# Performance work log

Measured on AMD Instinct MI355X. Metric: run time of the kernel, lower is better.

Reference implementation:

```python
import jax, jax.numpy as jnp
import numpy as np

B, S, D, H = 2, 2048, 1024, 16
HD = D // H  # 64


def setup_inputs() -> dict:
    key = jax.random.key(0)
    ks = jax.random.split(key, 7)
    std = 1.0 / np.sqrt(D)
    return {
        "q": jax.random.normal(ks[0], (B, S, D), jnp.float32),
        "k": jax.random.normal(ks[1], (B, S, D), jnp.float32),
        "v": jax.random.normal(ks[2], (B, S, D), jnp.float32),
        "w_q": jax.random.normal(ks[3], (D, D), jnp.float32) * std,
        "w_k": jax.random.normal(ks[4], (D, D), jnp.float32) * std,
        "w_v": jax.random.normal(ks[5], (D, D), jnp.float32) * std,
        "w_o": jax.random.normal(ks[6], (D, D), jnp.float32) * std,
    }


def reference(q, k, v, w_q, w_k, w_v, w_o):
    # Linear (torch nn.Linear, no bias): y = x @ W.T
    Q = jnp.einsum('bsd,ed->bse', q, w_q)
    K = jnp.einsum('bsd,ed->bse', k, w_k)
    V = jnp.einsum('bsd,ed->bse', v, w_v)
    # split heads -> (B, H, S, HD)
    Qh = Q.reshape(B, S, H, HD).transpose(0, 2, 1, 3)
    Kh = K.reshape(B, S, H, HD).transpose(0, 2, 1, 3)
    Vh = V.reshape(B, S, H, HD).transpose(0, 2, 1, 3)
    scale = 1.0 / np.sqrt(HD).astype(np.float32)
    scores = jnp.einsum('bhqd,bhkd->bhqk', Qh, Kh) * scale  # [B,H,S,S]
    attn = jax.nn.softmax(scores, axis=-1)
    ctx = jnp.einsum('bhqk,bhkd->bhqd', attn, Vh)
    combined = ctx.transpose(0, 2, 1, 3).reshape(B, S, D)
    out = jnp.einsum('bsd,ed->bse', combined, w_o)
    return out, attn
```

## Files before the change

### kernel.cpp

```cpp
#include <hip/hip_runtime.h>
#include <hip/hip_bf16.h>
#include <cstdint>

#define B_ 2
#define S_ 2048
#define D_ 1024
#define H_ 16
#define HD_ 64

#define SCALE_LOG2 0.18033688011112042f

typedef __attribute__((ext_vector_type(8))) __bf16 bf16x8;
typedef __attribute__((ext_vector_type(8))) unsigned short ushort8;
typedef __attribute__((ext_vector_type(4))) unsigned short ushort4v;
typedef __attribute__((ext_vector_type(4))) float f32x4;

__device__ __forceinline__ unsigned short f2bf(float f) {
  __bf16 h = (__bf16)f;
  return __builtin_bit_cast(unsigned short, h);
}

__device__ __forceinline__ float bf2f(unsigned short u) {
  union { unsigned int i; float f; } v; v.i = ((unsigned int)u) << 16; return v.f;
}

__device__ __forceinline__ float fexp2(float x) {
#if __has_builtin(__builtin_amdgcn_exp2f)
  return __builtin_amdgcn_exp2f(x);
#else
  return exp2f(x);
#endif
}

__device__ __forceinline__ f32x4 mfma16(bf16x8 a, bf16x8 b, f32x4 c) {
  return __builtin_amdgcn_mfma_f32_16x16x32_bf16(a, b, c, 0, 0, 0);
}

#define LGKM_BARRIER()                                        \
  do {                                                        \
    asm volatile("s_waitcnt lgkmcnt(0)" ::: "memory");        \
    __builtin_amdgcn_s_barrier();                             \
  } while (0)

__global__ __launch_bounds__(256) void proj_qkv_kernel(
    const float* __restrict__ qin, const float* __restrict__ kin,
    const float* __restrict__ vin, const float* __restrict__ wq,
    const float* __restrict__ wk, const float* __restrict__ wv,
    unsigned short* __restrict__ qh, unsigned short* __restrict__ kh,
    unsigned short* __restrict__ vt)
{
  __shared__ unsigned short As[128][40];
  __shared__ unsigned short Bs[128][40];

  const int z = blockIdx.z;
  const float* X = (z == 0) ? qin : (z == 1) ? kin : vin;
  const float* W = (z == 0) ? wq : (z == 1) ? wk : wv;
  unsigned short* dst = (z == 0) ? qh : (z == 1) ? kh : vt;
  const float osc = (z == 0) ? SCALE_LOG2 : 1.0f;

  const int lin = blockIdx.x + 8 * blockIdx.y;
  const int swz = (lin & 7) * 32 + (lin >> 3);
  const int bx = swz & 7, by = swz >> 3;

  const int tid = threadIdx.x;
  const int lane = tid & 63, wid = tid >> 6;
  const int c = lane & 15, g = lane >> 4;
  const int wr = wid >> 1, wc = wid & 1;
  const int m0 = by * 128, n0 = bx * 128;

  const int sr = tid >> 1, sh = tid & 1;
  const float* Ap = X + (size_t)(m0 + sr) * D_ + sh * 16;
  const float* Bp = W + (size_t)(n0 + sr) * D_ + sh * 16;

  float ar[16], br[16];
  f32x4 acc[4][4];
#pragma unroll
  for (int i = 0; i < 4; ++i)
#pragma unroll
    for (int j = 0; j < 4; ++j) acc[i][j] = (f32x4){0.f, 0.f, 0.f, 0.f};

  auto ldg_tile = [&](int kt) {
    const float* ap = Ap + kt * 32;
    const float* bp = Bp + kt * 32;
#pragma unroll
    for (int j = 0; j < 4; ++j) {
      *(f32x4*)(ar + 4 * j) = *(const f32x4*)(ap + 4 * j);
      *(f32x4*)(br + 4 * j) = *(const f32x4*)(bp + 4 * j);
    }
  };
  auto sts_tile = [&]() {
    unsigned short ta[16], tb[16];
#pragma unroll
    for (int j = 0; j < 16; ++j) { ta[j] = f2bf(ar[j]); tb[j] = f2bf(br[j]); }
    *(ushort8*)&As[sr][sh * 16]     = *(ushort8*)&ta[0];
    *(ushort8*)&As[sr][sh * 16 + 8] = *(ushort8*)&ta[8];
    *(ushort8*)&Bs[sr][sh * 16]     = *(ushort8*)&tb[0];
    *(ushort8*)&Bs[sr][sh * 16 + 8] = *(ushort8*)&tb[8];
  };

  ldg_tile(0);
  sts_tile();
  __syncthreads();

  for (int kt = 0; kt < 32; ++kt) {
    if (kt < 31) ldg_tile(kt + 1);
    bf16x8 af[4], bfr[4];
#pragma unroll
    for (int i = 0; i < 4; ++i) af[i]  = *(bf16x8*)&As[wr * 64 + i * 16 + c][g * 8];
#pragma unroll
    for (int i = 0; i < 4; ++i) bfr[i] = *(bf16x8*)&Bs[wc * 64 + i * 16 + c][g * 8];
#pragma unroll
    for (int mi = 0; mi < 4; ++mi)
#pragma unroll
      for (int ni = 0; ni < 4; ++ni)
        acc[mi][ni] = mfma16(af[mi], bfr[ni], acc[mi][ni]);
    __syncthreads();
    if (kt < 31) { sts_tile(); __syncthreads(); }
  }

#pragma unroll
  for (int mi = 0; mi < 4; ++mi) {
#pragma unroll
    for (int ni = 0; ni < 4; ++ni) {
      const int n = n0 + wc * 64 + ni * 16 + c;
      const int h = n >> 6, hd = n & 63;
      if (z < 2) {
#pragma unroll
        for (int r = 0; r < 4; ++r) {
          const int m = m0 + wr * 64 + mi * 16 + g * 4 + r;
          const int b = m >> 11, s = m & 2047;
          dst[((size_t)(b * H_ + h) * S_ + s) * HD_ + hd] = f2bf(acc[mi][ni][r] * osc);
        }
      } else {
        const int m = m0 + wr * 64 + mi * 16 + g * 4;
        const int b = m >> 11, s = m & 2047;
        ushort4v pk;
#pragma unroll
        for (int r = 0; r < 4; ++r) pk[r] = f2bf(acc[mi][ni][r]);
        *(ushort4v*)&dst[((size_t)(b * H_ + h) * HD_ + hd) * S_ + s] = pk;
      }
    }
  }
}

__global__ __launch_bounds__(256) void attn_kernel(
    const unsigned short* __restrict__ qh, const unsigned short* __restrict__ kh,
    const unsigned short* __restrict__ vt, float* __restrict__ attn,
    unsigned short* __restrict__ comb)
{
  __shared__ unsigned short Ks[64][72];
  __shared__ unsigned short Vs[64][72];
  __shared__ unsigned short Ps[4][16][88];

  const int tid = threadIdx.x;
  const int lane = tid & 63, w = tid >> 6;
  const int c = lane & 15, g = lane >> 4;

  const int lin = blockIdx.x;
  const int swz = (lin & 7) * 128 + (lin >> 3);
  const int bh = swz >> 5;
  const int q0 = (swz & 31) * 64;

  const unsigned short* Qb = qh + (size_t)bh * S_ * HD_;
  const unsigned short* Kb = kh + (size_t)bh * S_ * HD_;
  const unsigned short* Vb = vt + (size_t)bh * HD_ * S_;
  float* attnb = attn + (size_t)bh * S_ * S_;

  const int sr = tid >> 2;
  const int scol = (tid & 3) * 16;

  bf16x8 aQ[2];
#pragma unroll
  for (int t = 0; t < 2; ++t)
    aQ[t] = *(const bf16x8*)(Qb + (size_t)(q0 + w * 16 + c) * HD_ + t * 32 + g * 8);

  const unsigned short* Kst = Kb + (size_t)sr * HD_ + scol;
  const unsigned short* Vst = Vb + (size_t)sr * S_ + scol;

  float l = 0.f;
  ushort8 kr0 = *(const ushort8*)Kst;
  ushort8 kr1 = *(const ushort8*)(Kst + 8);

  for (int kt = 0; kt < 32; ++kt) {
    *(ushort8*)&Ks[sr][scol]     = kr0;
    *(ushort8*)&Ks[sr][scol + 8] = kr1;
    LGKM_BARRIER();
    if (kt < 31) {
      const unsigned short* p = Kst + (size_t)(kt + 1) * 64 * HD_;
      kr0 = *(const ushort8*)p;
      kr1 = *(const ushort8*)(p + 8);
    }
#pragma unroll
    for (int ni = 0; ni < 4; ++ni) {
      f32x4 a = (f32x4){0.f, 0.f, 0.f, 0.f};
      a = mfma16(*(bf16x8*)&Ks[ni * 16 + c][g * 8],      aQ[0], a);
      a = mfma16(*(bf16x8*)&Ks[ni * 16 + c][32 + g * 8], aQ[1], a);
      l += (fexp2(a[0]) + fexp2(a[1])) + (fexp2(a[2]) + fexp2(a[3]));
    }
    LGKM_BARRIER();
  }
  l += __shfl_xor(l, 16);
  l += __shfl_xor(l, 32);
  const float invl = 1.f / l;

  f32x4 ctx[4];
#pragma unroll
  for (int ni = 0; ni < 4; ++ni) ctx[ni] = (f32x4){0.f, 0.f, 0.f, 0.f};

  unsigned short* psrow = &Ps[w][c][g * 4];
  float* srow = attnb + (size_t)(q0 + w * 16 + g) * S_ + c * 4;

  kr0 = *(const ushort8*)Kst;
  kr1 = *(const ushort8*)(Kst + 8);
  ushort8 vr0 = *(const ushort8*)Vst;
  ushort8 vr1 = *(const ushort8*)(Vst + 8);

  for (int kt = 0; kt < 32; ++kt) {
    *(ushort8*)&Ks[sr][scol]     = kr0;
    *(ushort8*)&Ks[sr][scol + 8] = kr1;
    *(ushort8*)&Vs[sr][scol]     = vr0;
    *(ushort8*)&Vs[sr][scol + 8] = vr1;
    LGKM_BARRIER();
    if (kt < 31) {
      const unsigned short* p = Kst + (size_t)(kt + 1) * 64 * HD_;
      const unsigned short* q = Vst + (kt + 1) * 64;
      kr0 = *(const ushort8*)p;
      kr1 = *(const ushort8*)(p + 8);
      vr0 = *(const ushort8*)q;
      vr1 = *(const ushort8*)(q + 8);
    }

#pragma unroll
    for (int ni = 0; ni < 4; ++ni) {
      f32x4 a = (f32x4){0.f, 0.f, 0.f, 0.f};
      a = mfma16(*(bf16x8*)&Ks[ni * 16 + c][g * 8],      aQ[0], a);
      a = mfma16(*(bf16x8*)&Ks[ni * 16 + c][32 + g * 8], aQ[1], a);
      ushort4v pk;
#pragma unroll
      for (int r = 0; r < 4; ++r) pk[r] = f2bf(fexp2(a[r]) * invl);
      *(ushort4v*)(psrow + ni * 16) = pk;
    }

    bf16x8 aP[2];
#pragma unroll
    for (int t = 0; t < 2; ++t) aP[t] = *(bf16x8*)&Ps[w][c][t * 32 + g * 8];
#pragma unroll
    for (int ni = 0; ni < 4; ++ni)
#pragma unroll
      for (int t = 0; t < 2; ++t)
        ctx[ni] = mfma16(aP[t], *(bf16x8*)&Vs[ni * 16 + c][t * 32 + g * 8],
                         ctx[ni]);

#pragma unroll
    for (int it = 0; it < 4; ++it) {
      ushort4v pb = *(ushort4v*)&Ps[w][it * 4 + g][c * 4];
      f32x4 pf;
#pragma unroll
      for (int r = 0; r < 4; ++r) pf[r] = bf2f(pb[r]);
      __builtin_nontemporal_store(pf, (f32x4*)(srow + (size_t)it * 4 * S_ + kt * 64));
    }
    LGKM_BARRIER();
  }

  const int b = bh >> 4, h = bh & 15;
#pragma unroll
  for (int ni = 0; ni < 4; ++ni)
#pragma unroll
    for (int r = 0; r < 4; ++r)
      comb[(size_t)(b * S_ + q0 + w * 16 + g * 4 + r) * D_ + h * 64 + ni * 16 + c] =
          f2bf(ctx[ni][r]);
}

__global__ __launch_bounds__(256) void out_proj_kernel(
    const unsigned short* __restrict__ comb, const float* __restrict__ wo,
    float* __restrict__ out)
{
  __shared__ unsigned short As[128][40];
  __shared__ unsigned short Bs[128][40];

  const int lin = blockIdx.x + 8 * blockIdx.y;
  const int swz = (lin & 7) * 32 + (lin >> 3);
  const int bx = swz & 7, by = swz >> 3;

  const int tid = threadIdx.x;
  const int lane = tid & 63, wid = tid >> 6;
  const int c = lane & 15, g = lane >> 4;
  const int wr = wid >> 1, wc = wid & 1;
  const int m0 = by * 128, n0 = bx * 128;
  const int sr = tid >> 1, sh = tid & 1;

  const unsigned short* Apb = comb + (size_t)(m0 + sr) * D_ + sh * 16;
  const float* Bpb = wo + (size_t)(n0 + sr) * D_ + sh * 16;

  ushort8 ar2[2];
  float br[16];
  f32x4 acc[4][4];
#pragma unroll
  for (int i = 0; i < 4; ++i)
#pragma unroll
    for (int j = 0; j < 4; ++j) acc[i][j] = (f32x4){0.f, 0.f, 0.f, 0.f};

  auto ldg_tile = [&](int kt) {
    ar2[0] = *(const ushort8*)(Apb + kt * 32);
    ar2[1] = *(const ushort8*)(Apb + kt * 32 + 8);
#pragma unroll
    for (int j = 0; j < 4; ++j)
      *(f32x4*)(br + 4 * j) = *(const f32x4*)(Bpb + kt * 32 + 4 * j);
  };
  auto sts_tile = [&]() {
    *(ushort8*)&As[sr][sh * 16]     = ar2[0];
    *(ushort8*)&As[sr][sh * 16 + 8] = ar2[1];
    unsigned short tb[16];
#pragma unroll
    for (int j = 0; j < 16; ++j) tb[j] = f2bf(br[j]);
    *(ushort8*)&Bs[sr][sh * 16]     = *(ushort8*)&tb[0];
    *(ushort8*)&Bs[sr][sh * 16 + 8] = *(ushort8*)&tb[8];
  };

  ldg_tile(0);
  sts_tile();
  __syncthreads();

  for (int kt = 0; kt < 32; ++kt) {
    if (kt < 31) ldg_tile(kt + 1);
    bf16x8 af[4], bfr[4];
#pragma unroll
    for (int i = 0; i < 4; ++i) af[i]  = *(bf16x8*)&As[wr * 64 + i * 16 + c][g * 8];
#pragma unroll
    for (int i = 0; i < 4; ++i) bfr[i] = *(bf16x8*)&Bs[wc * 64 + i * 16 + c][g * 8];
#pragma unroll
    for (int mi = 0; mi < 4; ++mi)
#pragma unroll
      for (int ni = 0; ni < 4; ++ni)
        acc[mi][ni] = mfma16(af[mi], bfr[ni], acc[mi][ni]);
    __syncthreads();
    if (kt < 31) { sts_tile(); __syncthreads(); }
  }

#pragma unroll
  for (int mi = 0; mi < 4; ++mi)
#pragma unroll
    for (int ni = 0; ni < 4; ++ni)
#pragma unroll
      for (int r = 0; r < 4; ++r) {
        const int m = m0 + wr * 64 + mi * 16 + g * 4 + r;
        const int n = n0 + wc * 64 + ni * 16 + c;
        out[(size_t)m * D_ + n] = acc[mi][ni][r];
      }
}

extern "C" void kernel_launch(void* const* d_in, const int* in_sizes, int n_in,
                              void* d_out, int out_size, void* d_ws, size_t ws_size,
                              hipStream_t stream)
{
  const float* q  = (const float*)d_in[0];
  const float* k  = (const float*)d_in[1];
  const float* v  = (const float*)d_in[2];
  const float* wq = (const float*)d_in[3];
  const float* wk = (const float*)d_in[4];
  const float* wv = (const float*)d_in[5];
  const float* wo = (const float*)d_in[6];

  float* out  = (float*)d_out;
  float* attn = out + (size_t)B_ * S_ * D_;

  const size_t NE = (size_t)B_ * S_ * D_;
  unsigned short* qh   = (unsigned short*)d_ws;
  unsigned short* kh   = qh + NE;
  unsigned short* vt   = kh + NE;
  unsigned short* comb = vt + NE;

  proj_qkv_kernel<<<dim3(8, 32, 3), dim3(256), 0, stream>>>(q, k, v, wq, wk, wv, qh, kh, vt);
  attn_kernel<<<dim3(1024), dim3(256), 0, stream>>>(qh, kh, vt, attn, comb);
  out_proj_kernel<<<dim3(8, 32), dim3(256), 0, stream>>>(comb, wo, out);
}
```

Measured before the change: 232.1 us.

## Switch attention to 32x32x16 MFMA with 128-query tiles per block

The attention kernel now uses 32x32x16 bf16 MFMA instead of 16x16x32, so each wave handles 32 query rows and each block handles 128 queries. The grid is halved to 512 blocks, which doubles the reuse of every K/V tile loaded into LDS and lowers LDS read traffic per FLOP. In exchange each lane holds more accumulator registers, which may reduce occupancy, and there are fewer blocks to spread across CUs. The attn-matrix write-out loop now covers the 32 rows per wave.

```diff
diff --git a/kernel.cpp b/kernel.cpp
--- a/kernel.cpp
+++ b/kernel.cpp
@@ -14,6 +14,7 @@
 typedef __attribute__((ext_vector_type(8))) unsigned short ushort8;
 typedef __attribute__((ext_vector_type(4))) unsigned short ushort4v;
 typedef __attribute__((ext_vector_type(4))) float f32x4;
+typedef __attribute__((ext_vector_type(16))) float f32x16;
 
 __device__ __forceinline__ unsigned short f2bf(float f) {
   __bf16 h = (__bf16)f;
@@ -34,6 +35,9 @@
 
 __device__ __forceinline__ f32x4 mfma16(bf16x8 a, bf16x8 b, f32x4 c) {
   return __builtin_amdgcn_mfma_f32_16x16x32_bf16(a, b, c, 0, 0, 0);
+}
+__device__ __forceinline__ f32x16 mfma32(bf16x8 a, bf16x8 b, f32x16 c) {
+  return __builtin_amdgcn_mfma_f32_32x32x16_bf16(a, b, c, 0, 0, 0);
 }
 
 #define LGKM_BARRIER()                                        \
@@ -150,16 +154,18 @@
 {
   __shared__ unsigned short Ks[64][72];
   __shared__ unsigned short Vs[64][72];
-  __shared__ unsigned short Ps[4][16][88];
+  __shared__ unsigned short Ps[4][32][72];
 
   const int tid = threadIdx.x;
   const int lane = tid & 63, w = tid >> 6;
+  const int q32 = lane & 31, hi = lane >> 5;
   const int c = lane & 15, g = lane >> 4;
 
   const int lin = blockIdx.x;
-  const int swz = (lin & 7) * 128 + (lin >> 3);
-  const int bh = swz >> 5;
-  const int q0 = (swz & 31) * 64;
+  const int swz = (lin & 7) * 64 + (lin >> 3);
+  const int bh = swz >> 4;
+  const int q0 = (swz & 15) * 128;
+  const int qw = q0 + w * 32;
 
   const unsigned short* Qb = qh + (size_t)bh * S_ * HD_;
   const unsigned short* Kb = kh + (size_t)bh * S_ * HD_;
@@ -169,15 +175,15 @@
   const int sr = tid >> 2;
   const int scol = (tid & 3) * 16;
 
-  bf16x8 aQ[2];
-#pragma unroll
-  for (int t = 0; t < 2; ++t)
-    aQ[t] = *(const bf16x8*)(Qb + (size_t)(q0 + w * 16 + c) * HD_ + t * 32 + g * 8);
+  bf16x8 aQ[4];
+#pragma unroll
+  for (int t = 0; t < 4; ++t)
+    aQ[t] = *(const bf16x8*)(Qb + (size_t)(qw + q32) * HD_ + t * 16 + hi * 8);
 
   const unsigned short* Kst = Kb + (size_t)sr * HD_ + scol;
   const unsigned short* Vst = Vb + (size_t)sr * S_ + scol;
 
-  float l = 0.f;
+  float l4[4] = {0.f, 0.f, 0.f, 0.f};
   ushort8 kr0 = *(const ushort8*)Kst;
   ushort8 kr1 = *(const ushort8*)(Kst + 8);
 
@@ -191,24 +197,23 @@
       kr1 = *(const ushort8*)(p + 8);
     }
 #pragma unroll
-    for (int ni = 0; ni < 4; ++ni) {
-      f32x4 a = (f32x4){0.f, 0.f, 0.f, 0.f};
-      a = mfma16(*(bf16x8*)&Ks[ni * 16 + c][g * 8],      aQ[0], a);
-      a = mfma16(*(bf16x8*)&Ks[ni * 16 + c][32 + g * 8], aQ[1], a);
-      l += (fexp2(a[0]) + fexp2(a[1])) + (fexp2(a[2]) + fexp2(a[3]));
+    for (int kb = 0; kb < 2; ++kb) {
+      f32x16 p = (f32x16)(0.f);
+#pragma unroll
+      for (int t = 0; t < 4; ++t)
+        p = mfma32(*(bf16x8*)&Ks[kb * 32 + q32][t * 16 + hi * 8], aQ[t], p);
+#pragma unroll
+      for (int r = 0; r < 16; ++r) l4[r & 3] += fexp2(p[r]);
     }
     LGKM_BARRIER();
   }
-  l += __shfl_xor(l, 16);
+  float l = (l4[0] + l4[1]) + (l4[2] + l4[3]);
   l += __shfl_xor(l, 32);
   const float invl = 1.f / l;
 
-  f32x4 ctx[4];
-#pragma unroll
-  for (int ni = 0; ni < 4; ++ni) ctx[ni] = (f32x4){0.f, 0.f, 0.f, 0.f};
-
-  unsigned short* psrow = &Ps[w][c][g * 4];
-  float* srow = attnb + (size_t)(q0 + w * 16 + g) * S_ + c * 4;
+  f32x16 ctx0 = (f32x16)(0.f), ctx1 = (f32x16)(0.f);
+
+  float* srow = attnb + (size_t)(qw + g) * S_ + c * 4;
 
   kr0 = *(const ushort8*)Kst;
   kr1 = *(const ushort8*)(Kst + 8);
@@ -231,28 +236,32 @@
     }
 
 #pragma unroll
-    for (int ni = 0; ni < 4; ++ni) {
-      f32x4 a = (f32x4){0.f, 0.f, 0.f, 0.f};
-      a = mfma16(*(bf16x8*)&Ks[ni * 16 + c][g * 8],      aQ[0], a);
-      a = mfma16(*(bf16x8*)&Ks[ni * 16 + c][32 + g * 8], aQ[1], a);
-      ushort4v pk;
-#pragma unroll
-      for (int r = 0; r < 4; ++r) pk[r] = f2bf(fexp2(a[r]) * invl);
-      *(ushort4v*)(psrow + ni * 16) = pk;
-    }
-
-    bf16x8 aP[2];
-#pragma unroll
-    for (int t = 0; t < 2; ++t) aP[t] = *(bf16x8*)&Ps[w][c][t * 32 + g * 8];
-#pragma unroll
-    for (int ni = 0; ni < 4; ++ni)
-#pragma unroll
-      for (int t = 0; t < 2; ++t)
-        ctx[ni] = mfma16(aP[t], *(bf16x8*)&Vs[ni * 16 + c][t * 32 + g * 8],
-                         ctx[ni]);
-
-#pragma unroll
-    for (int it = 0; it < 4; ++it) {
+    for (int kb = 0; kb < 2; ++kb) {
+      f32x16 p = (f32x16)(0.f);
+#pragma unroll
+      for (int t = 0; t < 4; ++t)
+        p = mfma32(*(bf16x8*)&Ks[kb * 32 + q32][t * 16 + hi * 8], aQ[t], p);
+#pragma unroll
+      for (int j = 0; j < 4; ++j) {
+        ushort4v pk;
+#pragma unroll
+        for (int r = 0; r < 4; ++r) pk[r] = f2bf(fexp2(p[4 * j + r]) * invl);
+        *(ushort4v*)&Ps[w][q32][kb * 32 + 8 * j + 4 * hi] = pk;
+      }
+    }
+
+    bf16x8 pa[4];
+#pragma unroll
+    for (int t = 0; t < 4; ++t)
+      pa[t] = *(bf16x8*)&Ps[w][q32][t * 16 + hi * 8];
+#pragma unroll
+    for (int t = 0; t < 4; ++t) {
+      ctx0 = mfma32(pa[t], *(bf16x8*)&Vs[q32][t * 16 + hi * 8],      ctx0);
+      ctx1 = mfma32(pa[t], *(bf16x8*)&Vs[32 + q32][t * 16 + hi * 8], ctx1);
+    }
+
+#pragma unroll
+    for (int it = 0; it < 8; ++it) {
       ushort4v pb = *(ushort4v*)&Ps[w][it * 4 + g][c * 4];
       f32x4 pf;
 #pragma unroll
@@ -264,11 +273,12 @@
 
   const int b = bh >> 4, h = bh & 15;
 #pragma unroll
-  for (int ni = 0; ni < 4; ++ni)
-#pragma unroll
-    for (int r = 0; r < 4; ++r)
-      comb[(size_t)(b * S_ + q0 + w * 16 + g * 4 + r) * D_ + h * 64 + ni * 16 + c] =
-          f2bf(ctx[ni][r]);
+  for (int r = 0; r < 16; ++r) {
+    const int qrow = (r & 3) + 8 * (r >> 2) + 4 * hi;
+    unsigned short* cb = comb + (size_t)(b * S_ + qw + qrow) * D_ + h * 64 + q32;
+    cb[0]  = f2bf(ctx0[r]);
+    cb[32] = f2bf(ctx1[r]);
+  }
 }
 
 __global__ __launch_bounds__(256) void out_proj_kernel(
@@ -371,6 +381,6 @@
   unsigned short* comb = vt + NE;
 
   proj_qkv_kernel<<<dim3(8, 32, 3), dim3(256), 0, stream>>>(q, k, v, wq, wk, wv, qh, kh, vt);
-  attn_kernel<<<dim3(1024), dim3(256), 0, stream>>>(qh, kh, vt, attn, comb);
+  attn_kernel<<<dim3(512), dim3(256), 0, stream>>>(qh, kh, vt, attn, comb);
   out_proj_kernel<<<dim3(8, 32), dim3(256), 0, stream>>>(comb, wo, out);
 }
```

Measured after the change: 234.1 us. No clear change (+0.9%).
